# Optimization experiments

Measured on AMD Instinct MI355X. Metric: run time of the kernel, lower is better.

The kernel has to match this reference:

```python
import jax, jax.numpy as jnp
import numpy as np

P = 9  # patch_size


def setup_inputs() -> dict:
    key = jax.random.key(0)
    k1, k2 = jax.random.split(key)
    x = jax.random.normal(k1, (1, 4, 72, 72, 72), dtype=jnp.float32)
    # L = (72//9) * ((72*72)//9) = 8 * 576 = 4608
    attentions = jax.random.normal(k2, (1, 4, 4608, 4608), dtype=jnp.float32)
    return {"x": x, "attentions": attentions}


def reference(x, attentions):
    B, C, D, H, W = x.shape  # B == 1
    Hp, Wp = D, H * W
    x4 = x.reshape(1, C, Hp, Wp)  # [1, C, 72, 5184]
    nH, nW = Hp // P, Wp // P
    L = nH * nW

    # unfold (im2col), stride == kernel so it's a pure reshape/transpose:
    # cols[c, ki*P+kj, bi*nW+bj] = x4[0, c, bi*P+ki, bj*P+kj]
    patches = (
        x4[0]
        .reshape(C, nH, P, nW, P)
        .transpose(0, 2, 4, 1, 3)  # [C, P, P, nH, nW]
        .reshape(C, P * P, L)
    )

    attn = attentions[0]  # [C, L, L]
    # count_nonzero normalization (boolean mask -> no grad path, matches torch)
    nz = jnp.sum(attn != 0, axis=-1).astype(x.dtype)[..., None] + 1e-5  # [C, L, 1]
    attn_norm = attn / nz

    # att[c, l, k] = sum_m attn_norm[c, l, m] * patches[c, k, m]
    att = jnp.einsum("clm,ckm->clk", attn_norm, patches)  # [C, L, P*P]

    # fold (col2im), stride == kernel: inverse reshape/transpose
    corr = (
        att.transpose(0, 2, 1)  # [C, P*P, L]
        .reshape(C, P, P, nH, nW)
        .transpose(0, 3, 1, 4, 2)  # [C, nH, P, nW, P]
        .reshape(C, Hp, Wp)
    )[None]  # [1, C, Hp, Wp]

    out = corr * x4 + x4
    return jax.nn.leaky_relu(out, negative_slope=0.2)
```

## Files before the change

kernel.cpp:

```cpp
#include <hip/hip_runtime.h>
#include <stdint.h>

#define PSZ    9
#define CH     4
#define LROWS  4608
#define NWp    576
#define HPdim  72
#define WPdim  5184
#define NPAD   96
#define NVALID 81
#define KSPLIT 4
#define KSEG   (LROWS / KSPLIT)

typedef short s16x8 __attribute__((ext_vector_type(8)));
typedef float f32x4 __attribute__((ext_vector_type(4)));

__device__ __forceinline__ short f2bf(float f) {
    uint32_t u = __builtin_bit_cast(uint32_t, f);
    u += 0x8000u;
    return (short)(u >> 16);
}

__global__ __launch_bounds__(256) void build_pb_kernel(
    const float* __restrict__ x, uint16_t* __restrict__ pb)
{
    int tid = blockIdx.x * 256 + threadIdx.x;
    int m  = tid % LROWS;
    int cn = tid / LROWS;
    int n  = cn % NPAD;
    int c  = cn / NPAD;
    uint16_t v = 0;
    if (n < NVALID) {
        int ki = n / PSZ, kj = n % PSZ;
        int bi = m / NWp, bj = m % NWp;
        float f = x[(size_t)(c * HPdim + bi * PSZ + ki) * WPdim + bj * PSZ + kj];
        uint32_t u = __builtin_bit_cast(uint32_t, f);
        u += 0x8000u;
        v = (uint16_t)(u >> 16);
    }
    pb[tid] = v;
}

__global__ __launch_bounds__(256) void cross_gemm_kernel(
    const float* __restrict__ x,
    const float* __restrict__ attn,
    const uint16_t* __restrict__ pb,
    float* __restrict__ out)
{
    __shared__ float red[KSPLIT - 1][64][25];
    __shared__ int   cshared[KSPLIT][16];

    const int lane = threadIdx.x & 63;
    const int widx = threadIdx.x >> 6;
    const int blk  = blockIdx.x;
    const int c    = blk / 288;
    const int tile = blk - c * 288;
    const int r0   = tile * 16;
    const int li   = lane & 15;
    const int quad = lane >> 4;
    const int k0   = widx * KSEG;

    const float* aptr = attn + (size_t)(c * LROWS + r0 + li) * LROWS + k0 + quad * 8;
    const uint16_t* bptr = pb + (size_t)(c * NPAD + li) * LROWS + k0 + quad * 8;

    f32x4 acc[6];
#pragma unroll
    for (int t = 0; t < 6; ++t) acc[t] = (f32x4){0.f, 0.f, 0.f, 0.f};

    int cnt = 0;
    const int ITERS = KSEG / 32;

    float4 a0 = *(const float4*)(aptr);
    float4 a1 = *(const float4*)(aptr + 4);
    s16x8 b[6];
#pragma unroll
    for (int t = 0; t < 6; ++t)
        b[t] = *(const s16x8*)(bptr + t * 16 * LROWS);

    for (int it = 0; it < ITERS; ++it) {
        const int itn = (it + 1 < ITERS) ? (it + 1) : it;
        const float*    ap = aptr + itn * 32;
        const uint16_t* bp = bptr + itn * 32;
        float4 na0 = *(const float4*)(ap);
        float4 na1 = *(const float4*)(ap + 4);
        s16x8 nb[6];
#pragma unroll
        for (int t = 0; t < 6; ++t)
            nb[t] = *(const s16x8*)(bp + t * 16 * LROWS);

        cnt += (a0.x != 0.f) + (a0.y != 0.f) + (a0.z != 0.f) + (a0.w != 0.f)
             + (a1.x != 0.f) + (a1.y != 0.f) + (a1.z != 0.f) + (a1.w != 0.f);

        s16x8 af;
        af[0] = f2bf(a0.x); af[1] = f2bf(a0.y); af[2] = f2bf(a0.z); af[3] = f2bf(a0.w);
        af[4] = f2bf(a1.x); af[5] = f2bf(a1.y); af[6] = f2bf(a1.z); af[7] = f2bf(a1.w);

#pragma unroll
        for (int t = 0; t < 6; ++t)
            acc[t] = __builtin_amdgcn_mfma_f32_16x16x32_bf16(af, b[t], acc[t], 0, 0, 0);

        a0 = na0; a1 = na1;
#pragma unroll
        for (int t = 0; t < 6; ++t) b[t] = nb[t];
    }

    cnt += __shfl_down(cnt, 32);
    cnt += __shfl_down(cnt, 16);
    if (lane < 16) cshared[widx][lane] = cnt;

    if (widx > 0) {
#pragma unroll
        for (int t = 0; t < 6; ++t)
#pragma unroll
            for (int r = 0; r < 4; ++r)
                red[widx - 1][lane][t * 4 + r] = acc[t][r];
    }
    __syncthreads();

    if (widx == 0) {
#pragma unroll
        for (int reg = 0; reg < 4; ++reg) {
            const int lrow = quad * 4 + reg;
            const int cnt_r = cshared[0][lrow] + cshared[1][lrow]
                            + cshared[2][lrow] + cshared[3][lrow];
            const float scale = 1.0f / ((float)cnt_r + 1e-5f);
            const int l  = r0 + lrow;
            const int bi = l / NWp;
            const int bj = l - bi * NWp;
#pragma unroll
            for (int t = 0; t < 6; ++t) {
                const int n = t * 16 + li;
                if (n < NVALID) {
                    const float v = acc[t][reg]
                                  + red[0][lane][t * 4 + reg]
                                  + red[1][lane][t * 4 + reg]
                                  + red[2][lane][t * 4 + reg];
                    const int ki = n / PSZ, kj = n - (n / PSZ) * PSZ;
                    const size_t idx = (size_t)(c * HPdim + bi * PSZ + ki) * WPdim
                                     + (size_t)(bj * PSZ + kj);
                    const float xv = x[idx];
                    const float o  = xv * (1.0f + v * scale);
                    out[idx] = (o > 0.f) ? o : 0.2f * o;
                }
            }
        }
    }
}

extern "C" void kernel_launch(void* const* d_in, const int* in_sizes, int n_in,
                              void* d_out, int out_size, void* d_ws, size_t ws_size,
                              hipStream_t stream)
{
    const float* x    = (const float*)d_in[0];
    const float* attn = (const float*)d_in[1];
    float* out        = (float*)d_out;
    uint16_t* pb      = (uint16_t*)d_ws;

    const int total_pb = CH * NPAD * LROWS;
    build_pb_kernel<<<total_pb / 256, 256, 0, stream>>>(x, pb);
    cross_gemm_kernel<<<CH * 288, 256, 0, stream>>>(x, attn, pb, out);
}
```

Baseline: 574.7 us.

## Block patch matrix into K-tiles and stage x through shared memory

The bf16 patch matrix is now stored as contiguous 32-wide K blocks of 96x32 elements, so each GEMM iteration reads one compact 6 KB tile instead of 96 rows strided by the full L. The build kernel loads a 9x288 slab of x into LDS and writes each tile with coalesced stores, replacing the scattered per-element gathers. The main cost is still the fp32 attention stream, so any benefit is limited to B-operand locality and the prep kernel.

After: 504.2 us. 1.14x faster.

```diff
diff --git a/kernel.cpp b/kernel.cpp
--- a/kernel.cpp
+++ b/kernel.cpp
@@ -11,34 +11,45 @@
 #define NVALID 81
 #define KSPLIT 4
 #define KSEG   (LROWS / KSPLIT)
+#define KBLK   32
+#define NKB    (LROWS / KBLK)
 
 typedef short s16x8 __attribute__((ext_vector_type(8)));
 typedef float f32x4 __attribute__((ext_vector_type(4)));
 
-__device__ __forceinline__ short f2bf(float f) {
+__device__ __forceinline__ uint16_t f2bf(float f) {
     uint32_t u = __builtin_bit_cast(uint32_t, f);
     u += 0x8000u;
-    return (short)(u >> 16);
+    return (uint16_t)(u >> 16);
 }
 
 __global__ __launch_bounds__(256) void build_pb_kernel(
     const float* __restrict__ x, uint16_t* __restrict__ pb)
 {
-    int tid = blockIdx.x * 256 + threadIdx.x;
-    int m  = tid % LROWS;
-    int cn = tid / LROWS;
-    int n  = cn % NPAD;
-    int c  = cn / NPAD;
-    uint16_t v = 0;
-    if (n < NVALID) {
-        int ki = n / PSZ, kj = n % PSZ;
-        int bi = m / NWp, bj = m % NWp;
-        float f = x[(size_t)(c * HPdim + bi * PSZ + ki) * WPdim + bj * PSZ + kj];
-        uint32_t u = __builtin_bit_cast(uint32_t, f);
-        u += 0x8000u;
-        v = (uint16_t)(u >> 16);
+    __shared__ float xs[PSZ][288];
+    const int blk = blockIdx.x;
+    const int c   = blk / NKB;
+    const int kb  = blk - c * NKB;
+    const int bi  = kb / 18;
+    const int bj0 = (kb - bi * 18) * KBLK;
+
+    const float* src = x + (size_t)(c * HPdim + bi * PSZ) * WPdim + bj0 * PSZ;
+    for (int idx = threadIdx.x; idx < PSZ * 288; idx += 256) {
+        int r = idx / 288, col = idx - r * 288;
+        xs[r][col] = src[(size_t)r * WPdim + col];
     }
-    pb[tid] = v;
+    __syncthreads();
+
+    uint16_t* dst = pb + (size_t)(c * NKB + kb) * NPAD * KBLK;
+    for (int oidx = threadIdx.x; oidx < NPAD * KBLK; oidx += 256) {
+        int n = oidx / KBLK, ks = oidx - n * KBLK;
+        uint16_t v = 0;
+        if (n < NVALID) {
+            int ki = n / PSZ, kj = n - ki * PSZ;
+            v = f2bf(xs[ki][ks * PSZ + kj]);
+        }
+        dst[oidx] = v;
+    }
 }
 
 __global__ __launch_bounds__(256) void cross_gemm_kernel(
@@ -59,9 +70,11 @@
     const int li   = lane & 15;
     const int quad = lane >> 4;
     const int k0   = widx * KSEG;
+    const int kb0  = k0 / KBLK;
 
     const float* aptr = attn + (size_t)(c * LROWS + r0 + li) * LROWS + k0 + quad * 8;
-    const uint16_t* bptr = pb + (size_t)(c * NPAD + li) * LROWS + k0 + quad * 8;
+    const uint16_t* bbase = pb + (size_t)(c * NKB + kb0) * NPAD * KBLK
+                          + li * KBLK + quad * 8;
 
     f32x4 acc[6];
 #pragma unroll
@@ -75,18 +88,18 @@
     s16x8 b[6];
 #pragma unroll
     for (int t = 0; t < 6; ++t)
-        b[t] = *(const s16x8*)(bptr + t * 16 * LROWS);
+        b[t] = *(const s16x8*)(bbase + t * 16 * KBLK);
 
     for (int it = 0; it < ITERS; ++it) {
         const int itn = (it + 1 < ITERS) ? (it + 1) : it;
         const float*    ap = aptr + itn * 32;
-        const uint16_t* bp = bptr + itn * 32;
+        const uint16_t* bp = bbase + (size_t)itn * NPAD * KBLK;
         float4 na0 = *(const float4*)(ap);
         float4 na1 = *(const float4*)(ap + 4);
         s16x8 nb[6];
 #pragma unroll
         for (int t = 0; t < 6; ++t)
-            nb[t] = *(const s16x8*)(bp + t * 16 * LROWS);
+            nb[t] = *(const s16x8*)(bp + t * 16 * KBLK);
 
         cnt += (a0.x != 0.f) + (a0.y != 0.f) + (a0.z != 0.f) + (a0.w != 0.f)
              + (a1.x != 0.f) + (a1.y != 0.f) + (a1.z != 0.f) + (a1.w != 0.f);
@@ -156,7 +169,6 @@
     float* out        = (float*)d_out;
     uint16_t* pb      = (uint16_t*)d_ws;
 
-    const int total_pb = CH * NPAD * LROWS;
-    build_pb_kernel<<<total_pb / 256, 256, 0, stream>>>(x, pb);
+    build_pb_kernel<<<CH * NKB, 256, 0, stream>>>(x, pb);
     cross_gemm_kernel<<<CH * 288, 256, 0, stream>>>(x, attn, pb, out);
 }
```
